# Kernel tuning notes

Measured on AMD Instinct MI355X. Metric: run time of the kernel, lower is better.

Reference implementation:

```python
import jax, jax.numpy as jnp
import numpy as np

B, C, H, W = 4, 256, 64, 64
C8 = C // 8


def setup_inputs() -> dict:
    key = jax.random.key(0)
    ks = jax.random.split(key, 8)
    s = 1.0 / np.sqrt(C)
    return {
        "x_ccd": jax.random.normal(ks[0], (B, C, H, W), jnp.float32),
        "x_dem": jax.random.normal(ks[1], (B, C, H, W), jnp.float32),
        "Wq": jax.random.normal(ks[2], (C8, C), jnp.float32) * s,
        "bq": jax.random.normal(ks[3], (C8,), jnp.float32) * 0.01,
        "Wk": jax.random.normal(ks[4], (C8, C), jnp.float32) * s,
        "bk": jax.random.normal(ks[5], (C8,), jnp.float32) * 0.01,
        "Wv": jax.random.normal(ks[6], (C, C), jnp.float32) * s,
        "bv": jax.random.normal(ks[7], (C,), jnp.float32) * 0.01,
        "gamma": jnp.zeros((1,), jnp.float32),
    }


def reference(x_ccd, x_dem, Wq, bq, Wk, bk, Wv, bv, gamma):
    b, c, h, w = x_ccd.shape
    n = h * w
    xc = x_ccd.reshape(b, c, n)  # [B,C,N]
    xd = x_dem.reshape(b, c, n)
    # 1x1 convs == per-pixel linear projections
    q = jnp.einsum("oc,bcn->bno", Wq, xc) + bq  # [B,N,C8]
    k = jnp.einsum("oc,bcn->bon", Wk, xd) + bk[None, :, None]  # [B,C8,N]
    energy = jnp.einsum("bno,bom->bnm", q, k)  # [B,N,N]
    attention = jax.nn.softmax(energy, axis=-1)
    v = jnp.einsum("oc,bcn->bon", Wv, xd) + bv[None, :, None]  # [B,C,N]
    out = jnp.einsum("bom,bnm->bon", v, attention)  # value @ attention^T
    out = out.reshape(b, c, h, w)
    return gamma * out + x_ccd
```

## Files before the change

kernel.cpp:

```cpp
#include <hip/hip_runtime.h>

typedef unsigned short u16;
typedef unsigned int u32;
typedef short v8s __attribute__((ext_vector_type(8)));
typedef float v16f __attribute__((ext_vector_type(16)));
typedef unsigned int v2u __attribute__((ext_vector_type(2)));

#define MFMA(a, b, c) __builtin_amdgcn_mfma_f32_32x32x16_bf16(a, b, c, 0, 0, 0)
#define L2E 1.44269504088896f

union U8 { v8s s; uint4 u4; u32 u[4]; };

__device__ __forceinline__ u16 f2bf(float x) {
    u32 u = __float_as_uint(x);
    return (u16)((u + 0x7FFFu + ((u >> 16) & 1u)) >> 16);
}
__device__ __forceinline__ u32 pk2(float a, float b) {
    return (u32)f2bf(a) | ((u32)f2bf(b) << 16);
}
__device__ __forceinline__ u32 pkz(float e0, float e1) {
    return __builtin_amdgcn_perm(__float_as_uint(e1), __float_as_uint(e0), 0x07060302u);
}


__global__ __launch_bounds__(256) void prep_w_kernel(
    const float* __restrict__ Wq, const float* __restrict__ bq,
    const float* __restrict__ Wk, const float* __restrict__ bk,
    const float* __restrict__ Wv, const float* __restrict__ bv,
    u16* __restrict__ WfT, float* __restrict__ ball)
{
    int tid = blockIdx.x * 256 + threadIdx.x;
    if (tid < 81920) {
        int ch = tid >> 8, c = tid & 255;
        float w;
        if (ch < 32)      w = Wq[ch * 256 + c];
        else if (ch < 64) w = Wk[(ch - 32) * 256 + c] * L2E;
        else              w = Wv[(ch - 64) * 256 + c];
        int tile = (ch >> 5) * 16 + (c >> 4);
        int lane = ((c >> 3) & 1) * 32 + (ch & 31);
        WfT[tile * 512 + lane * 8 + (c & 7)] = f2bf(w);
    } else if (tid < 82240) {
        int i = tid - 81920;
        float bb;
        if (i < 32)      bb = bq[i];
        else if (i < 64) bb = bk[i - 32] * L2E;
        else             bb = bv[i - 64];
        ball[i] = bb;
    }
}

__global__ __launch_bounds__(256, 2) void proj_kernel(
    const float* __restrict__ xc, const float* __restrict__ xd,
    const u16* __restrict__ WfT, const float* __restrict__ ball,
    u16* __restrict__ qfT, u16* __restrict__ kfT, u16* __restrict__ vfT)
{
    __shared__ u16 xls[2][32][264];
    int blk = blockIdx.x, b = blk >> 7, n0 = (blk & 127) * 32;
    int t = threadIdx.x, lane = t & 63, wv = t >> 6;
    int hl = lane >> 5, l31 = lane & 31;

#pragma unroll
    for (int p = 0; p < 4; p++) {
        int s = p * 256 + t;
        int arr = s >> 9, c4 = (s >> 3) & 63, n4s = s & 7;
        const float* src = arr ? xd : xc;
        size_t g0 = ((size_t)(b * 256 + c4 * 4)) * 4096 + n0 + n4s * 4;
        float4 r0 = *(const float4*)&src[g0];
        float4 r1 = *(const float4*)&src[g0 + 4096];
        float4 r2 = *(const float4*)&src[g0 + 8192];
        float4 r3 = *(const float4*)&src[g0 + 12288];
        *(uint2*)&xls[arr][n4s * 4 + 0][c4 * 4] = make_uint2(pk2(r0.x, r1.x), pk2(r2.x, r3.x));
        *(uint2*)&xls[arr][n4s * 4 + 1][c4 * 4] = make_uint2(pk2(r0.y, r1.y), pk2(r2.y, r3.y));
        *(uint2*)&xls[arr][n4s * 4 + 2][c4 * 4] = make_uint2(pk2(r0.z, r1.z), pk2(r2.z, r3.z));
        *(uint2*)&xls[arr][n4s * 4 + 3][c4 * 4] = make_uint2(pk2(r0.w, r1.w), pk2(r2.w, r3.w));
    }
    __syncthreads();

    int jobs[3];
    int nj;
    if (wv == 0)      { jobs[0] = 0; jobs[1] = 2; jobs[2] = 0; nj = 2; }
    else if (wv == 1) { jobs[0] = 1; jobs[1] = 3; jobs[2] = 0; nj = 2; }
    else if (wv == 2) { jobs[0] = 4; jobs[1] = 5; jobs[2] = 6; nj = 3; }
    else              { jobs[0] = 7; jobs[1] = 8; jobs[2] = 9; nj = 3; }

    int nt = blk & 127;
    int n = n0 + l31;
    int vl = ((n >> 3) & 1) * 32, tk = n >> 4, j8 = n & 7;

    for (int jj = 0; jj < nj; jj++) {
        int j = jobs[jj];
        int arr = (j != 0);
        const u16* wb = WfT + (size_t)(j * 16) * 512 + lane * 8;
        v16f acc = {};
#pragma unroll
        for (int kc = 0; kc < 16; kc++) {
            U8 bx, a;
            bx.u4 = *(const uint4*)&xls[arr][l31][kc * 16 + hl * 8];
            a.u4  = *(const uint4*)(wb + (size_t)kc * 512);
            acc = MFMA(a.s, bx.s, acc);
        }
        if (j <= 1) {
            u16* dst = j ? kfT : qfT;
#pragma unroll
            for (int i = 0; i < 8; i++) {
                int r = 2 * i;
                int row = (r & 3) + 8 * (r >> 2) + 4 * hl;
                float b0 = ball[j * 32 + row], b1 = ball[j * 32 + row + 1];
                u32 st = pk2(acc[r] + b0, acc[r + 1] + b1);
                size_t off = (((size_t)(b * 128 + nt) * 2 + (row >> 4)) * 512)
                           + (((row >> 3) & 1) * 32 + l31) * 8 + (row & 7);
                *(u32*)&dst[off] = st;
            }
        } else {
            int vi = j - 2;
            u16* vdst = vfT + (((size_t)(b * 8 + vi) * 256 + tk) * 512) + vl * 8 + j8;
#pragma unroll
            for (int r = 0; r < 16; r++) {
                int row = (r & 3) + 8 * (r >> 2) + 4 * hl;
                vdst[row * 8] = f2bf(acc[r] + ball[64 + vi * 32 + row]);
            }
        }
    }
}

__global__ __launch_bounds__(512, 4) void flash_kernel(
    const u16* __restrict__ qfT, const u16* __restrict__ kfT,
    const u16* __restrict__ vfT, const float* __restrict__ xccd,
    const float* __restrict__ gptr, float* __restrict__ outp)
{
    __shared__ float red[4][2][16][64];
    __shared__ float lred[2][32];

    const int t = threadIdx.x, lane = t & 63, wv = t >> 6;
    const int hl = lane >> 5, l31 = lane & 31;
    const int blk = blockIdx.x;
    const int b = (blk & 7) >> 1;
    const int qt = ((blk >> 3) << 1) | (blk & 1);
    const int kh = wv & 1, chq = wv >> 1;
    const int n0 = qt * 32;

    U8 qf0, qf1;
    {
        const u16* qp = qfT + ((size_t)(b * 128 + qt) * 2) * 512 + lane * 8;
        qf0.u4 = *(const uint4*)qp;
        qf1.u4 = *(const uint4*)(qp + 512);
    }

    v16f acc[2] = {};
    float lrun = 0.f;

    const u16* kp = kfT + ((size_t)(b * 128 + kh)) * 1024 + lane * 8;
    const u16* vp = vfT + (((size_t)(b * 8 + chq * 2) * 256) + 2 * kh) * 512 + lane * 8;

    U8 k0[2], k1[2], v0[2][2], v1[2][2];

    auto load_frags = [&](U8 (&kf)[2], U8 (&vf)[2][2], int it) {
        const u16* k = kp + (size_t)it * 2048;
        kf[0].u4 = *(const uint4*)k;
        kf[1].u4 = *(const uint4*)(k + 512);
        const u16* v = vp + (size_t)it * 2048;
        vf[0][0].u4 = *(const uint4*)v;
        vf[0][1].u4 = *(const uint4*)(v + 512);
        vf[1][0].u4 = *(const uint4*)(v + 131072);
        vf[1][1].u4 = *(const uint4*)(v + 131072 + 512);
    };

    auto step = [&](U8 (&kf)[2], U8 (&vf)[2][2]) {
        v16f E = {};
        E = MFMA(kf[0].s, qf0.s, E);
        E = MFMA(kf[1].s, qf1.s, E);
        u32 pkv[8];
#pragma unroll
        for (int j = 0; j < 8; j++)
            pkv[j] = pkz(__builtin_amdgcn_exp2f(E[2 * j]),
                         __builtin_amdgcn_exp2f(E[2 * j + 1]));
        if (chq == 0) {
            float sl = 0.f;
#pragma unroll
            for (int j = 0; j < 8; j++) {
                sl += __uint_as_float(pkv[j] & 0xFFFF0000u);
                sl += __uint_as_float(pkv[j] << 16);
            }
            lrun += sl;
        }
        U8 B0, B1;
        {
            v2u r;
            r = __builtin_amdgcn_permlane32_swap(pkv[0], pkv[2], 0, 0); B0.u[0] = r[0]; B0.u[2] = r[1];
            r = __builtin_amdgcn_permlane32_swap(pkv[1], pkv[3], 0, 0); B0.u[1] = r[0]; B0.u[3] = r[1];
            r = __builtin_amdgcn_permlane32_swap(pkv[4], pkv[6], 0, 0); B1.u[0] = r[0]; B1.u[2] = r[1];
            r = __builtin_amdgcn_permlane32_swap(pkv[5], pkv[7], 0, 0); B1.u[1] = r[0]; B1.u[3] = r[1];
        }
        __builtin_amdgcn_s_setprio(1);
        acc[0] = MFMA(vf[0][0].s, B0.s, acc[0]);
        acc[0] = MFMA(vf[0][1].s, B1.s, acc[0]);
        acc[1] = MFMA(vf[1][0].s, B0.s, acc[1]);
        acc[1] = MFMA(vf[1][1].s, B1.s, acc[1]);
        __builtin_amdgcn_s_setprio(0);
    };

    load_frags(k0, v0, 0);
#pragma unroll 1
    for (int it = 0; it < 64; it += 2) {
        load_frags(k1, v1, it + 1);
        step(k0, v0);
        if (it + 2 < 64) load_frags(k0, v0, it + 2);
        step(k1, v1);
    }

    if (kh == 1) {
#pragma unroll
        for (int ct = 0; ct < 2; ct++)
#pragma unroll
            for (int r = 0; r < 16; r++)
                red[chq][ct][r][lane] = acc[ct][r];
    }
    if (chq == 0) {
        v2u rr = __builtin_amdgcn_permlane32_swap(__float_as_uint(lrun),
                                                  __float_as_uint(lrun), 0, 0);
        float ltot = __uint_as_float(rr[0]) + __uint_as_float(rr[1]);
        if (lane < 32) lred[kh][l31] = ltot;
    }
    __syncthreads();
    if (kh == 0) {
        const float g = gptr[0];
        const float sc = g / (lred[0][l31] + lred[1][l31]);
#pragma unroll
        for (int ct = 0; ct < 2; ct++)
#pragma unroll
            for (int r = 0; r < 16; r++) {
                float v = acc[ct][r] + red[chq][ct][r][lane];
                int ch = chq * 64 + ct * 32 + (r & 3) + 8 * (r >> 2) + 4 * hl;
                size_t ga = ((size_t)(b * 256 + ch)) * 4096 + n0 + l31;
                outp[ga] = v * sc + xccd[ga];
            }
    }
}

extern "C" void kernel_launch(void* const* d_in, const int* in_sizes, int n_in,
                              void* d_out, int out_size, void* d_ws, size_t ws_size,
                              hipStream_t stream)
{
    const float* xc    = (const float*)d_in[0];
    const float* xd    = (const float*)d_in[1];
    const float* Wq    = (const float*)d_in[2];
    const float* bq    = (const float*)d_in[3];
    const float* Wk    = (const float*)d_in[4];
    const float* bk    = (const float*)d_in[5];
    const float* Wv    = (const float*)d_in[6];
    const float* bv    = (const float*)d_in[7];
    const float* gamma = (const float*)d_in[8];
    float* out = (float*)d_out;

    u16* qfT  = (u16*)d_ws;
    u16* kfT  = qfT + (size_t)524288;
    u16* vfT  = kfT + (size_t)524288;
    u16* WfT  = vfT + (size_t)4194304;
    float* bl = (float*)(WfT + 81920);

    prep_w_kernel<<<322, 256, 0, stream>>>(Wq, bq, Wk, bk, Wv, bv, WfT, bl);
    proj_kernel<<<512, 256, 0, stream>>>(xc, xd, WfT, bl, qfT, kfT, vfT);
    flash_kernel<<<512, 512, 0, stream>>>(qfT, kfT, vfT, xc, gamma, out);
}
```

Baseline: 173.1 us.

## Share softmax probabilities across waves via LDS instead of recomputing per wave

Previously every wave recomputed QK^T and exp for its key half, so the four channel-quarter waves duplicated the softmax work. Now each of the 8 waves computes P for a distinct key tile and writes it to a double-buffered LDS array. Each wave then consumes four tiles for its channel quarter and key half, with block-wide barriers per stage. This removes the redundant MFMA and exp work at the cost of LDS traffic, a __syncthreads per stage, and a restructured register pipeline.

```diff
diff --git a/kernel.cpp b/kernel.cpp
--- a/kernel.cpp
+++ b/kernel.cpp
@@ -123,20 +123,25 @@
     }
 }
 
+union ShU {
+    u32   P[2][8][2][64][4];
+    float red[4][2][16][64];
+};
+
 __global__ __launch_bounds__(512, 4) void flash_kernel(
     const u16* __restrict__ qfT, const u16* __restrict__ kfT,
     const u16* __restrict__ vfT, const float* __restrict__ xccd,
     const float* __restrict__ gptr, float* __restrict__ outp)
 {
-    __shared__ float red[4][2][16][64];
-    __shared__ float lred[2][32];
+    __shared__ ShU sh;
+    __shared__ float lred[8][32];
 
     const int t = threadIdx.x, lane = t & 63, wv = t >> 6;
     const int hl = lane >> 5, l31 = lane & 31;
     const int blk = blockIdx.x;
-    const int b = (blk & 7) >> 1;
+    const int b  = (blk & 7) >> 1;
     const int qt = ((blk >> 3) << 1) | (blk & 1);
-    const int kh = wv & 1, chq = wv >> 1;
+    const int kq = wv >> 2, chq = wv & 3;
     const int n0 = qt * 32;
 
     U8 qf0, qf1;
@@ -149,87 +154,124 @@
     v16f acc[2] = {};
     float lrun = 0.f;
 
-    const u16* kp = kfT + ((size_t)(b * 128 + kh)) * 1024 + lane * 8;
-    const u16* vp = vfT + (((size_t)(b * 8 + chq * 2) * 256) + 2 * kh) * 512 + lane * 8;
-
-    U8 k0[2], k1[2], v0[2][2], v1[2][2];
-
-    auto load_frags = [&](U8 (&kf)[2], U8 (&vf)[2][2], int it) {
-        const u16* k = kp + (size_t)it * 2048;
-        kf[0].u4 = *(const uint4*)k;
-        kf[1].u4 = *(const uint4*)(k + 512);
-        const u16* v = vp + (size_t)it * 2048;
-        vf[0][0].u4 = *(const uint4*)v;
-        vf[0][1].u4 = *(const uint4*)(v + 512);
-        vf[1][0].u4 = *(const uint4*)(v + 131072);
-        vf[1][1].u4 = *(const uint4*)(v + 131072 + 512);
-    };
-
-    auto step = [&](U8 (&kf)[2], U8 (&vf)[2][2]) {
+    const u16* kp = kfT + ((size_t)(b * 128 + wv)) * 1024 + lane * 8;
+    const u16* vp = vfT + ((size_t)(b * 8 + chq * 2) * 256) * 512 + lane * 8;
+
+    U8 kb0[2], kb1[2];
+    kb0[0].u4 = *(const uint4*)(kp);
+    kb0[1].u4 = *(const uint4*)(kp + 512);
+    kb1[0].u4 = *(const uint4*)(kp + 8192);
+    kb1[1].u4 = *(const uint4*)(kp + 8192 + 512);
+
+    auto produce = [&](U8 (&kb)[2], int buf) {
         v16f E = {};
-        E = MFMA(kf[0].s, qf0.s, E);
-        E = MFMA(kf[1].s, qf1.s, E);
+        E = MFMA(kb[0].s, qf0.s, E);
+        E = MFMA(kb[1].s, qf1.s, E);
         u32 pkv[8];
 #pragma unroll
         for (int j = 0; j < 8; j++)
             pkv[j] = pkz(__builtin_amdgcn_exp2f(E[2 * j]),
                          __builtin_amdgcn_exp2f(E[2 * j + 1]));
-        if (chq == 0) {
-            float sl = 0.f;
-#pragma unroll
-            for (int j = 0; j < 8; j++) {
-                sl += __uint_as_float(pkv[j] & 0xFFFF0000u);
-                sl += __uint_as_float(pkv[j] << 16);
-            }
-            lrun += sl;
-        }
+        float sl = 0.f;
+#pragma unroll
+        for (int j = 0; j < 8; j++) {
+            sl += __uint_as_float(pkv[j] & 0xFFFF0000u);
+            sl += __uint_as_float(pkv[j] << 16);
+        }
+        lrun += sl;
         U8 B0, B1;
+        v2u r;
+        r = __builtin_amdgcn_permlane32_swap(pkv[0], pkv[2], 0, 0); B0.u[0] = r[0]; B0.u[2] = r[1];
+        r = __builtin_amdgcn_permlane32_swap(pkv[1], pkv[3], 0, 0); B0.u[1] = r[0]; B0.u[3] = r[1];
+        r = __builtin_amdgcn_permlane32_swap(pkv[4], pkv[6], 0, 0); B1.u[0] = r[0]; B1.u[2] = r[1];
+        r = __builtin_amdgcn_permlane32_swap(pkv[5], pkv[7], 0, 0); B1.u[1] = r[0]; B1.u[3] = r[1];
+        *(uint4*)&sh.P[buf][wv][0][lane][0] = B0.u4;
+        *(uint4*)&sh.P[buf][wv][1][lane][0] = B1.u4;
+    };
+
+    produce(kb0, 0);
+    __syncthreads();
+
+    const int tb = kq * 4;
+#pragma unroll 1
+    for (int s = 0; s < 16; s++) {
+        const int cb = s & 1, nb = cb ^ 1;
+        const int t0 = s * 8 + tb;
+        U8 bA0, bA1, bB0, bB1;
+        bA0.u4 = *(const uint4*)&sh.P[cb][tb][0][lane][0];
+        bA1.u4 = *(const uint4*)&sh.P[cb][tb][1][lane][0];
+        U8 vA[2][2], vB[2][2];
         {
-            v2u r;
-            r = __builtin_amdgcn_permlane32_swap(pkv[0], pkv[2], 0, 0); B0.u[0] = r[0]; B0.u[2] = r[1];
-            r = __builtin_amdgcn_permlane32_swap(pkv[1], pkv[3], 0, 0); B0.u[1] = r[0]; B0.u[3] = r[1];
-            r = __builtin_amdgcn_permlane32_swap(pkv[4], pkv[6], 0, 0); B1.u[0] = r[0]; B1.u[2] = r[1];
-            r = __builtin_amdgcn_permlane32_swap(pkv[5], pkv[7], 0, 0); B1.u[1] = r[0]; B1.u[3] = r[1];
-        }
-        __builtin_amdgcn_s_setprio(1);
-        acc[0] = MFMA(vf[0][0].s, B0.s, acc[0]);
-        acc[0] = MFMA(vf[0][1].s, B1.s, acc[0]);
-        acc[1] = MFMA(vf[1][0].s, B0.s, acc[1]);
-        acc[1] = MFMA(vf[1][1].s, B1.s, acc[1]);
-        __builtin_amdgcn_s_setprio(0);
-    };
-
-    load_frags(k0, v0, 0);
-#pragma unroll 1
-    for (int it = 0; it < 64; it += 2) {
-        load_frags(k1, v1, it + 1);
-        step(k0, v0);
-        if (it + 2 < 64) load_frags(k0, v0, it + 2);
-        step(k1, v1);
-    }
-
-    if (kh == 1) {
-#pragma unroll
-        for (int ct = 0; ct < 2; ct++)
-#pragma unroll
-            for (int r = 0; r < 16; r++)
-                red[chq][ct][r][lane] = acc[ct][r];
-    }
-    if (chq == 0) {
+            const u16* v0p = vp + (size_t)(2 * t0) * 512;
+            vA[0][0].u4 = *(const uint4*)(v0p);
+            vA[0][1].u4 = *(const uint4*)(v0p + 512);
+            vA[1][0].u4 = *(const uint4*)(v0p + 131072);
+            vA[1][1].u4 = *(const uint4*)(v0p + 131072 + 512);
+        }
+        if (s < 15) {
+            if ((s & 1) == 0) {
+                produce(kb1, nb);
+                if (s < 14) {
+                    kb0[0].u4 = *(const uint4*)(kp + (size_t)(s + 2) * 8192);
+                    kb0[1].u4 = *(const uint4*)(kp + (size_t)(s + 2) * 8192 + 512);
+                }
+            } else {
+                produce(kb0, nb);
+                if (s < 14) {
+                    kb1[0].u4 = *(const uint4*)(kp + (size_t)(s + 2) * 8192);
+                    kb1[1].u4 = *(const uint4*)(kp + (size_t)(s + 2) * 8192 + 512);
+                }
+            }
+        }
+#pragma unroll
+        for (int j = 0; j < 4; j++) {
+            if (j < 3) {
+                bB0.u4 = *(const uint4*)&sh.P[cb][tb + j + 1][0][lane][0];
+                bB1.u4 = *(const uint4*)&sh.P[cb][tb + j + 1][1][lane][0];
+                const u16* vnp = vp + (size_t)(2 * (t0 + j + 1)) * 512;
+                vB[0][0].u4 = *(const uint4*)(vnp);
+                vB[0][1].u4 = *(const uint4*)(vnp + 512);
+                vB[1][0].u4 = *(const uint4*)(vnp + 131072);
+                vB[1][1].u4 = *(const uint4*)(vnp + 131072 + 512);
+            }
+            __builtin_amdgcn_s_setprio(1);
+            acc[0] = MFMA(vA[0][0].s, bA0.s, acc[0]);
+            acc[0] = MFMA(vA[0][1].s, bA1.s, acc[0]);
+            acc[1] = MFMA(vA[1][0].s, bA0.s, acc[1]);
+            acc[1] = MFMA(vA[1][1].s, bA1.s, acc[1]);
+            __builtin_amdgcn_s_setprio(0);
+            bA0 = bB0; bA1 = bB1;
+            vA[0][0] = vB[0][0]; vA[0][1] = vB[0][1];
+            vA[1][0] = vB[1][0]; vA[1][1] = vB[1][1];
+        }
+        __syncthreads();
+    }
+
+    {
         v2u rr = __builtin_amdgcn_permlane32_swap(__float_as_uint(lrun),
                                                   __float_as_uint(lrun), 0, 0);
         float ltot = __uint_as_float(rr[0]) + __uint_as_float(rr[1]);
-        if (lane < 32) lred[kh][l31] = ltot;
+        if (lane < 32) lred[wv][l31] = ltot;
+    }
+    if (kq == 1) {
+#pragma unroll
+        for (int ct = 0; ct < 2; ct++)
+#pragma unroll
+            for (int r = 0; r < 16; r++)
+                sh.red[chq][ct][r][lane] = acc[ct][r];
     }
     __syncthreads();
-    if (kh == 0) {
+    if (kq == 0) {
+        float lsum = 0.f;
+#pragma unroll
+        for (int w = 0; w < 8; w++) lsum += lred[w][l31];
         const float g = gptr[0];
-        const float sc = g / (lred[0][l31] + lred[1][l31]);
+        const float sc = g / lsum;
 #pragma unroll
         for (int ct = 0; ct < 2; ct++)
 #pragma unroll
             for (int r = 0; r < 16; r++) {
-                float v = acc[ct][r] + red[chq][ct][r][lane];
+                float v = acc[ct][r] + sh.red[chq][ct][r][lane];
                 int ch = chq * 64 + ct * 32 + (r & 3) + 8 * (r >> 2) + 4 * hl;
                 size_t ga = ((size_t)(b * 256 + ch)) * 4096 + n0 + l31;
                 outp[ga] = v * sc + xccd[ga];
```

After: 155.1 us. -10.4%, faster.
